# Kernel optimization log

Measured on AMD Instinct MI355X. Metric: run time of the kernel, lower is better.

## Reference

```python
import jax, jax.numpy as jnp
import numpy as np

B, T, C = 2, 2048, 2048
NH = 16          # n_head
G = 4            # group_size
NKV = NH // G    # kv heads
HD = C // NH     # head_dim = 128
BASE = 10000.0


def setup_inputs() -> dict:
    key = jax.random.key(0)
    ks = jax.random.split(key, 9)
    s = 0.02
    return {
        "x": jax.random.normal(ks[0], (B, T, C), jnp.float32),
        "wq_w": jax.random.normal(ks[1], (C, C), jnp.float32) * s,
        "wq_b": jax.random.normal(ks[2], (C,), jnp.float32) * s,
        "wk_w": jax.random.normal(ks[3], (C // G, C), jnp.float32) * s,
        "wk_b": jax.random.normal(ks[4], (C // G,), jnp.float32) * s,
        "wv_w": jax.random.normal(ks[5], (C // G, C), jnp.float32) * s,
        "wv_b": jax.random.normal(ks[6], (C // G,), jnp.float32) * s,
        "cp_w": jax.random.normal(ks[7], (C, C), jnp.float32) * s,
        "cp_b": jax.random.normal(ks[8], (C,), jnp.float32) * s,
    }


def _rope(x):
    # Faithful to source: RoPE is applied to [B, H, T, HD] but the module
    # reads seq_len = x.size(1) == H, so the rotation angle is indexed by the
    # HEAD axis and broadcast over sequence positions.
    b, h, t, d = x.shape
    half = d // 2
    theta = 1.0 / (BASE ** (jnp.arange(0, half, dtype=jnp.float32) * 2.0 / d))  # [half]
    ang = jnp.arange(h, dtype=jnp.float32)[:, None] * theta[None, :]            # [h, half]
    cos = jnp.cos(ang)[None, :, None, :]  # [1, h, 1, half]
    sin = jnp.sin(ang)[None, :, None, :]
    xs = x.reshape(b, h, t, half, 2)
    x0, x1 = xs[..., 0], xs[..., 1]
    out = jnp.stack([x0 * cos - x1 * sin, x1 * cos + x0 * sin], axis=-1)
    return out.reshape(b, h, t, d)


def reference(x, wq_w, wq_b, wk_w, wk_b, wv_w, wv_b, cp_w, cp_b):
    b, t, c = x.shape
    q = x @ wq_w.T + wq_b                                  # [B,T,C]
    k = x @ wk_w.T + wk_b                                  # [B,T,C//G]
    v = x @ wv_w.T + wv_b                                  # [B,T,C//G]
    q = q.reshape(b, t, NH, HD).transpose(0, 2, 1, 3)      # [B,NH,T,HD]
    k = k.reshape(b, t, NKV, HD).transpose(0, 2, 1, 3)     # [B,NKV,T,HD]
    v = v.reshape(b, t, NKV, HD).transpose(0, 2, 1, 3)
    q = _rope(q)
    k = _rope(k)
    # GQA expand: each kv head repeated G times consecutively
    k = jnp.repeat(k, G, axis=1)                           # [B,NH,T,HD]
    v = jnp.repeat(v, G, axis=1)
    att = jnp.einsum('bhqd,bhkd->bhqk', q, k) / (HD ** 0.5)
    mask = jnp.tril(jnp.ones((t, t), dtype=bool))
    att = jnp.where(mask[None, None], att, -jnp.inf)
    att = jax.nn.softmax(att, axis=-1)
    y = jnp.einsum('bhqk,bhkd->bhqd', att, v)
    y = y.transpose(0, 2, 1, 3).reshape(b, t, c)
    return y @ cp_w.T + cp_b
```

## Files before the change

### kernel.cpp

```cpp
#include <hip/hip_runtime.h>

typedef unsigned short u16;
typedef __bf16 bf16x8 __attribute__((ext_vector_type(8)));
typedef float f32x4 __attribute__((ext_vector_type(4)));
typedef float f32x16 __attribute__((ext_vector_type(16)));
typedef unsigned u32x4 __attribute__((ext_vector_type(4)));

#define T_   2048
#define C_   2048
#define HD_  128
#define NH_  16
#define NKV_ 4
#define M_   4096

typedef __attribute__((address_space(1))) const void* as1_cvp;
typedef __attribute__((address_space(3))) void* as3_vp;

__device__ __forceinline__ void gload16(const void* g, void* l) {
  __builtin_amdgcn_global_load_lds((as1_cvp)g, (as3_vp)l, 16, 0, 0);
}

__device__ __forceinline__ u16 f2bf(float f) {
  unsigned u = __builtin_bit_cast(unsigned, f);
  return (u16)((u + 0x7fffu + ((u >> 16) & 1u)) >> 16);
}

__device__ __forceinline__ float fexp2(float x) {
  float r;
  asm("v_exp_f32 %0, %1" : "=v"(r) : "v"(x));
  return r;
}

__device__ __forceinline__ unsigned cvtpk(float a, float b) {
  unsigned d;
  asm("v_cvt_pk_bf16_f32 %0, %1, %2" : "=v"(d) : "v"(a), "v"(b));
  return d;
}

__global__ void cvt_bf16(const float4* __restrict__ in, ushort4* __restrict__ out, int n4) {
  int i = blockIdx.x * blockDim.x + threadIdx.x;
  if (i >= n4) return;
  float4 v = in[i];
  ushort4 r;
  r.x = f2bf(v.x); r.y = f2bf(v.y); r.z = f2bf(v.z); r.w = f2bf(v.w);
  out[i] = r;
}

__global__ void copy_f32(const float* __restrict__ in, float* __restrict__ out, int n) {
  int i = blockIdx.x * blockDim.x + threadIdx.x;
  if (i < n) out[i] = in[i];
}

__global__ void rope_fold_w(const float* __restrict__ W, u16* __restrict__ out, int npair) {
  int idx = blockIdx.x * blockDim.x + threadIdx.x;
  int p  = idx >> 9;
  int c4 = (idx & 511) << 2;
  if (p >= npair) return;
  int h  = p >> 6;
  int ii = p & 63;
  float theta = __expf(-(float)ii * (9.210340371976184f / 64.0f));
  float s, c;
  __sincosf((float)h * theta, &s, &c);
  size_t r0 = (size_t)(2 * p) * 2048 + c4;
  size_t r1 = r0 + 2048;
  float4 a = *(const float4*)(W + r0);
  float4 b = *(const float4*)(W + r1);
  ushort4 o0, o1;
  o0.x = f2bf(a.x * c - b.x * s); o0.y = f2bf(a.y * c - b.y * s);
  o0.z = f2bf(a.z * c - b.z * s); o0.w = f2bf(a.w * c - b.w * s);
  o1.x = f2bf(b.x * c + a.x * s); o1.y = f2bf(b.y * c + a.y * s);
  o1.z = f2bf(b.z * c + a.z * s); o1.w = f2bf(b.w * c + a.w * s);
  *(ushort4*)(out + r0) = o0;
  *(ushort4*)(out + r1) = o1;
}

__global__ void rope_fold_b(const float* __restrict__ bin, float* __restrict__ bout, int npair) {
  int p = blockIdx.x * blockDim.x + threadIdx.x;
  if (p >= npair) return;
  int h = p >> 6, ii = p & 63;
  float theta = __expf(-(float)ii * (9.210340371976184f / 64.0f));
  float s, c;
  __sincosf((float)h * theta, &s, &c);
  float a = bin[2 * p], b = bin[2 * p + 1];
  bout[2 * p]     = a * c - b * s;
  bout[2 * p + 1] = b * c + a * s;
}

template<int BN, int MODE>
__global__ __launch_bounds__(512)
void gemm10(const u16* __restrict__ A, const u16* __restrict__ W,
            const float* __restrict__ bias, void* __restrict__ op0,
            void* __restrict__ op1, void* __restrict__ op2, const float qscale) {
  constexpr int NREP = BN / 32;
  constexpr int ABUF = 16384;
  constexpr int BBUF = BN * 64;
  constexpr int NBL  = BN / 64;
  __shared__ __align__(16) u16 sm[3 * ABUF + 2 * BBUF];
  const int tid  = threadIdx.x;
  const int lane = tid & 63;
  const int wid  = tid >> 6;
  const int wr = wid >> 1, wc = wid & 1;
  const int m0 = blockIdx.y << 8;
  const int n0 = blockIdx.x * BN;
  const int K  = C_;
  const int fr = lane & 15, g = lane >> 4;
  const int rs0 = ((g ^ (fr & 7)) << 3);
  const int rs1 = (((4 + g) ^ (fr & 7)) << 3);

  size_t sofA[4]; int sdstA[4];
#pragma unroll
  for (int l = 0; l < 4; ++l) {
    const int j = l * 512 + tid, rl = j >> 3, sl = j & 7;
    sofA[l] = (size_t)rl * K + ((sl ^ (rl & 7)) << 3);
    sdstA[l] = j * 8;
  }
  size_t sofB[NBL]; int sdstB[NBL];
#pragma unroll
  for (int l = 0; l < NBL; ++l) {
    const int j = l * 512 + tid, rl = j >> 3, sl = j & 7;
    sofB[l] = (size_t)rl * K + ((sl ^ (rl & 7)) << 3);
    sdstB[l] = j * 8;
  }
  const u16* Ab = A + (size_t)m0 * K;
  const u16* Bb = W + (size_t)n0 * K;

  f32x4 acc[4][NREP] = {};

#define SA(l, ks, buf) gload16(Ab + (size_t)(ks) * 64 + sofA[l], sm + (buf) * ABUF + sdstA[l]);
#define SB(l, ks, buf) gload16(Bb + (size_t)(ks) * 64 + sofB[l], sm + 3 * ABUF + (buf) * BBUF + sdstB[l]);
#define LDA(RS) { _Pragma("unroll")                                       \
  for (int mi = 0; mi < 4; ++mi) {                                        \
    const int row = wr * 64 + mi * 16 + fr;                               \
    af[mi] = *(const bf16x8*)&sm[ab + row * 64 + (RS)]; } }
#define LDB(RS) { _Pragma("unroll")                                       \
  for (int ni = 0; ni < NREP; ++ni) {                                     \
    const int row = wc * (BN / 2) + ni * 16 + fr;                         \
    bq[ni] = *(const bf16x8*)&sm[3 * ABUF + bb + row * 64 + (RS)]; } }
#define MMQ { __builtin_amdgcn_s_setprio(1); _Pragma("unroll")            \
  for (int mi = 0; mi < 4; ++mi) _Pragma("unroll")                        \
    for (int ni = 0; ni < NREP; ++ni)                                     \
      acc[mi][ni] = __builtin_amdgcn_mfma_f32_16x16x32_bf16(              \
          af[mi], bq[ni], acc[mi][ni], 0, 0, 0);                          \
  __builtin_amdgcn_s_setprio(0); }
#define LGKM0 { asm volatile("s_waitcnt lgkmcnt(0)" ::: "memory");        \
                __builtin_amdgcn_sched_barrier(0); }

#pragma unroll
  for (int l = 0; l < NBL; ++l) SB(l, 0, 0)
#pragma unroll
  for (int l = 0; l < 4; ++l) SA(l, 0, 0)
#pragma unroll
  for (int l = 0; l < 4; ++l) SA(l, 1, 1)
  asm volatile("s_waitcnt vmcnt(4)" ::: "memory");
  __builtin_amdgcn_s_barrier();

  int a0 = 0, a2 = 2;
  for (int s = 0; s < 32; ++s) {
    const int ab = a0 * ABUF;
    const int bb = (s & 1) * BBUF;
    const int b1 = (s & 1) ^ 1;
    bf16x8 af[4], bq[NREP];
    LDB(rs0) LDA(rs0)
    if (s < 31) {
#pragma unroll
      for (int l = 0; l < NBL; ++l) SB(l, s + 1, b1)
    }
    __builtin_amdgcn_s_barrier();
    LGKM0
    MMQ
    __builtin_amdgcn_s_barrier();
    LDB(rs1) LDA(rs1)
    if (s < 30) {
#pragma unroll
      for (int l = 0; l < 4; ++l) SA(l, s + 2, a2)
      asm volatile("s_waitcnt vmcnt(4)" ::: "memory");
    } else if (s == 30) {
      asm volatile("s_waitcnt vmcnt(0)" ::: "memory");
    }
    __builtin_amdgcn_s_barrier();
    LGKM0
    MMQ
    __builtin_amdgcn_s_barrier();
    a0 = (a0 == 2) ? 0 : a0 + 1;
    a2 = (a2 == 2) ? 0 : a2 + 1;
  }
#undef SA
#undef SB
#undef LDA
#undef LDB
#undef MMQ
#undef LGKM0

#pragma unroll
  for (int mi = 0; mi < 4; ++mi) {
    const int rg0 = m0 + wr * 64 + mi * 16 + ((lane >> 4) << 2);
#pragma unroll
    for (int ni = 0; ni < NREP; ++ni) {
      const int cg = n0 + wc * (BN / 2) + ni * 16 + fr;
      const float bb2 = bias[cg];
#pragma unroll
      for (int r = 0; r < 4; ++r) {
        float v = acc[mi][ni][r] + bb2;
        const int rg = rg0 + r;
        if (MODE == 1) {
          ((float*)op0)[(size_t)rg * C_ + cg] = v;
        } else {
          const int b = rg >> 11, t = rg & (T_ - 1);
          if (cg < 2048) {
            const int h = cg >> 7, d = cg & 127;
            ((u16*)op0)[((((size_t)b * NH_ + h) * T_ + t) << 7) + d] = f2bf(v * qscale);
          } else if (cg < 2560) {
            const int c2 = cg - 2048, h = c2 >> 7, d = c2 & 127;
            ((u16*)op1)[((((size_t)b * NKV_ + h) * T_ + t) << 7) + d] = f2bf(v);
          } else {
            const int c2 = cg - 2560, h = c2 >> 7, d = c2 & 127;
            ((u16*)op2)[(((size_t)b * NKV_ + h) * HD_ + d) * T_ + t] = f2bf(v);
          }
        }
      }
    }
  }
}

__device__ __forceinline__ void stage_kv(u16* dst, const u16* __restrict__ kg,
                                         const u16* __restrict__ vg, int lane, int w) {
#pragma unroll
  for (int r = 0; r < 4; ++r) {
    const int row = r * 16 + w * 4 + (lane >> 4);
    const int cg  = (lane & 15) ^ (row & 7);
    gload16(kg + (size_t)row * 128 + cg * 8, dst + row * 128 + (lane & 15) * 8);
  }
#pragma unroll
  for (int r = 0; r < 4; ++r) {
    const int row = r * 32 + w * 8 + (lane >> 3);
    const int cg  = (lane & 7) ^ (row & 7);
    gload16(vg + (size_t)row * T_ + cg * 8, dst + 8192 + row * 64 + (lane & 7) * 8);
  }
}

__global__ __launch_bounds__(256, 2)
void attn2(const u16* __restrict__ q, const u16* __restrict__ k,
           const u16* __restrict__ vt, u16* __restrict__ y) {
  __shared__ __align__(16) u16 sm[32768];
  const int tid  = threadIdx.x;
  const int lane = tid & 63;
  const int w    = tid >> 6;
  const int hi   = lane >> 5;
  const int l5   = lane & 31;
  const int h = blockIdx.y;
  const int b = blockIdx.z;
  const int qt = b ? (int)blockIdx.x : (15 - (int)blockIdx.x);
  const int q0  = qt << 7;
  const int q0w = q0 + w * 32;
  const int nkv = 2 * qt + 2;
  const size_t qbase = (((size_t)b * NH_ + h) * T_ + q0) * HD_;
  const size_t kbase = ((size_t)b * NKV_ + (h >> 2)) * (size_t)T_ * HD_;
  const size_t vbase = ((size_t)b * NKV_ + (h >> 2)) * (size_t)HD_ * T_;

#pragma unroll
  for (int r = 0; r < 8; ++r) {
    const int row = r * 16 + w * 4 + (lane >> 4);
    const int cg  = (lane & 15) ^ (row & 7);
    gload16(q + qbase + (size_t)row * 128 + cg * 8, sm + row * 128 + (lane & 15) * 8);
  }
  __syncthreads();
  bf16x8 qf[8];
  {
    const int row = w * 32 + l5;
#pragma unroll
    for (int kd = 0; kd < 8; ++kd)
      qf[kd] = *(const bf16x8*)&sm[row * 128 + ((((kd << 1) | hi) ^ (row & 7)) << 3)];
  }
  __syncthreads();
  stage_kv(sm, k + kbase, vt + vbase, lane, w);

  f32x16 o[4] = {};
  float m = -1e30f, l = 0.f;

  for (int kv = 0; kv < nkv; ++kv) {
    __syncthreads();
    const int buf = kv & 1;
    if (kv + 1 < nkv)
      stage_kv(sm + ((buf ^ 1) << 14),
               k + kbase + ((size_t)(kv + 1) << 6) * 128,
               vt + vbase + ((kv + 1) << 6), lane, w);

    if ((kv << 6) <= q0w + 31) {
      const u16* Ks = sm + (buf << 14);
      const u16* Vs = Ks + 8192;

      f32x16 st[2] = {};
      __builtin_amdgcn_s_setprio(1);
#pragma unroll
      for (int kt = 0; kt < 2; ++kt) {
        const int krow = kt * 32 + l5;
#pragma unroll
        for (int kd = 0; kd < 8; ++kd) {
          bf16x8 ka = *(const bf16x8*)&Ks[krow * 128 + ((((kd << 1) | hi) ^ (l5 & 7)) << 3)];
          st[kt] = __builtin_amdgcn_mfma_f32_32x32x16_bf16(ka, qf[kd], st[kt], 0, 0, 0);
        }
      }
      __builtin_amdgcn_s_setprio(0);

      if ((kv << 6) + 63 > q0w) {
        const int qg = q0w + l5;
#pragma unroll
        for (int kt = 0; kt < 2; ++kt)
#pragma unroll
          for (int r = 0; r < 16; ++r) {
            const int kg = (kv << 6) + kt * 32 + (r & 3) + ((r >> 2) << 3) + (hi << 2);
            if (kg > qg) st[kt][r] = -3.0e38f;
          }
      }

      float pmax = -3.0e38f;
#pragma unroll
      for (int kt = 0; kt < 2; ++kt)
#pragma unroll
        for (int r = 0; r < 16; ++r) pmax = fmaxf(pmax, st[kt][r]);
      pmax = fmaxf(pmax, __shfl_xor(pmax, 32));
      if (!__all(pmax - m <= 8.0f)) {
        const float mn = fmaxf(m, pmax);
        const float f = fexp2(m - mn);
        m = mn;
        l *= f;
#pragma unroll
        for (int r = 0; r < 16; ++r) {
          const float fr = __shfl(f, (r & 3) + ((r >> 2) << 3) + (hi << 2));
          o[0][r] *= fr; o[1][r] *= fr; o[2][r] *= fr; o[3][r] *= fr;
        }
      }

      float rs = 0.f;
#pragma unroll
      for (int kt = 0; kt < 2; ++kt) {
#pragma unroll
        for (int s = 0; s < 2; ++s) {
          float e0 = fexp2(st[kt][8 * s + 0] - m), e1 = fexp2(st[kt][8 * s + 1] - m);
          float e2 = fexp2(st[kt][8 * s + 2] - m), e3 = fexp2(st[kt][8 * s + 3] - m);
          float e4 = fexp2(st[kt][8 * s + 4] - m), e5 = fexp2(st[kt][8 * s + 5] - m);
          float e6 = fexp2(st[kt][8 * s + 6] - m), e7 = fexp2(st[kt][8 * s + 7] - m);
          rs += ((e0 + e1) + (e2 + e3)) + ((e4 + e5) + (e6 + e7));
          const unsigned wL0 = cvtpk(e0, e1), wL1 = cvtpk(e2, e3);
          const unsigned wH0 = cvtpk(e4, e5), wH1 = cvtpk(e6, e7);
          const unsigned s0 = hi ? wL0 : wH0, s1 = hi ? wL1 : wH1;
          const unsigned r0 = __shfl_xor(s0, 32), r1 = __shfl_xor(s1, 32);
          u32x4 fw;
          fw.x = hi ? r0 : wL0; fw.y = hi ? r1 : wL1;
          fw.z = hi ? wH0 : r0; fw.w = hi ? wH1 : r1;
          const bf16x8 pa = __builtin_bit_cast(bf16x8, fw);
          const int ch = (((kt * 2 + s) << 1) | hi) ^ (l5 & 7);
          __builtin_amdgcn_s_setprio(1);
#pragma unroll
          for (int ds = 0; ds < 4; ++ds) {
            const int vrow = ds * 32 + l5;
            bf16x8 vb = *(const bf16x8*)&Vs[vrow * 64 + (ch << 3)];
            o[ds] = __builtin_amdgcn_mfma_f32_32x32x16_bf16(pa, vb, o[ds], 0, 0, 0);
          }
          __builtin_amdgcn_s_setprio(0);
        }
      }
      rs += __shfl_xor(rs, 32);
      l += rs;
    }
  }

  const float linv = 1.0f / l;
#pragma unroll
  for (int r = 0; r < 16; ++r) {
    const int crow = (r & 3) + ((r >> 2) << 3) + (hi << 2);
    const float lf = __shfl(linv, crow);
    const int qg = q0w + crow;
    const size_t rowoff = (((size_t)(b << 11) + qg) << 11) + (h << 7) + l5;
#pragma unroll
    for (int ds = 0; ds < 4; ++ds)
      y[rowoff + ds * 32] = f2bf(o[ds][r] * lf);
  }
}

extern "C" void kernel_launch(void* const* d_in, const int* in_sizes, int n_in,
                              void* d_out, int out_size, void* d_ws, size_t ws_size,
                              hipStream_t stream) {
  (void)in_sizes; (void)n_in; (void)out_size; (void)ws_size;
  const float* x    = (const float*)d_in[0];
  const float* wq_w = (const float*)d_in[1];
  const float* wq_b = (const float*)d_in[2];
  const float* wk_w = (const float*)d_in[3];
  const float* wk_b = (const float*)d_in[4];
  const float* wv_w = (const float*)d_in[5];
  const float* wv_b = (const float*)d_in[6];
  const float* cp_w = (const float*)d_in[7];
  const float* cp_b = (const float*)d_in[8];

  char* ws = (char*)d_ws;
  u16* xb  = (u16*)ws;  ws += (size_t)M_ * C_ * 2;
  u16* wqr = (u16*)ws;  ws += (size_t)C_ * C_ * 2;
  u16* wkr = (u16*)ws;  ws += (size_t)512 * C_ * 2;
  u16* wvb = (u16*)ws;  ws += (size_t)512 * C_ * 2;
  u16* cpb = (u16*)ws;  ws += (size_t)C_ * C_ * 2;
  u16* qb  = (u16*)ws;  ws += (size_t)M_ * C_ * 2;
  u16* kb  = (u16*)ws;  ws += (size_t)M_ * 512 * 2;
  u16* vtb = (u16*)ws;  ws += (size_t)M_ * 512 * 2;
  float* bqkv = (float*)ws; ws += 3072 * 4;
  u16* yb = xb;

  cvt_bf16<<<8192, 256, 0, stream>>>((const float4*)x,    (ushort4*)xb,  2097152);
  cvt_bf16<<<1024, 256, 0, stream>>>((const float4*)wv_w, (ushort4*)wvb, 262144);
  cvt_bf16<<<4096, 256, 0, stream>>>((const float4*)cp_w, (ushort4*)cpb, 1048576);
  rope_fold_w<<<2048, 256, 0, stream>>>(wq_w, wqr, 1024);
  rope_fold_w<<<512,  256, 0, stream>>>(wk_w, wkr, 256);
  rope_fold_b<<<4, 256, 0, stream>>>(wq_b, bqkv, 1024);
  rope_fold_b<<<1, 256, 0, stream>>>(wk_b, bqkv + 2048, 256);
  copy_f32<<<2, 256, 0, stream>>>(wv_b, bqkv + 2560, 512);

  const float qscale = 0.08838834764831843f * 1.4426950408889634f;
  gemm10<192, 0><<<dim3(16, 16), 512, 0, stream>>>(xb, wqr, bqkv, qb, kb, vtb, qscale);

  attn2<<<dim3(16, 16, 2), 256, 0, stream>>>(qb, kb, vtb, yb);

  gemm10<128, 1><<<dim3(16, 16), 512, 0, stream>>>(yb, cpb, cp_b, (float*)d_out,
                                                   nullptr, nullptr, 1.0f);
}
```

Baseline: 191.2 us.

## Load both k-halves per stage and use one barrier per GEMM iteration

The GEMM main loop now reads both 32-wide k-halves of the A and B fragments from LDS up front, issues the next global→LDS prefetches, then runs all MFMAs for the stage. The vmcnt wait and a single workgroup barrier move to the end of the iteration, replacing the four barriers and two lgkmcnt waits per iteration. The aim is to cut synchronisation stalls and let LDS reads overlap MFMA work. In exchange it doubles the live fragment registers, which could raise VGPR pressure or cause spills.

```diff
diff --git a/kernel.cpp b/kernel.cpp
--- a/kernel.cpp
+++ b/kernel.cpp
@@ -88,7 +88,7 @@
 
 template<int BN, int MODE>
 __global__ __launch_bounds__(512)
-void gemm10(const u16* __restrict__ A, const u16* __restrict__ W,
+void gemm11(const u16* __restrict__ A, const u16* __restrict__ W,
             const float* __restrict__ bias, void* __restrict__ op0,
             void* __restrict__ op1, void* __restrict__ op2, const float qscale) {
   constexpr int NREP = BN / 32;
@@ -128,22 +128,6 @@
 
 #define SA(l, ks, buf) gload16(Ab + (size_t)(ks) * 64 + sofA[l], sm + (buf) * ABUF + sdstA[l]);
 #define SB(l, ks, buf) gload16(Bb + (size_t)(ks) * 64 + sofB[l], sm + 3 * ABUF + (buf) * BBUF + sdstB[l]);
-#define LDA(RS) { _Pragma("unroll")                                       \
-  for (int mi = 0; mi < 4; ++mi) {                                        \
-    const int row = wr * 64 + mi * 16 + fr;                               \
-    af[mi] = *(const bf16x8*)&sm[ab + row * 64 + (RS)]; } }
-#define LDB(RS) { _Pragma("unroll")                                       \
-  for (int ni = 0; ni < NREP; ++ni) {                                     \
-    const int row = wc * (BN / 2) + ni * 16 + fr;                         \
-    bq[ni] = *(const bf16x8*)&sm[3 * ABUF + bb + row * 64 + (RS)]; } }
-#define MMQ { __builtin_amdgcn_s_setprio(1); _Pragma("unroll")            \
-  for (int mi = 0; mi < 4; ++mi) _Pragma("unroll")                        \
-    for (int ni = 0; ni < NREP; ++ni)                                     \
-      acc[mi][ni] = __builtin_amdgcn_mfma_f32_16x16x32_bf16(              \
-          af[mi], bq[ni], acc[mi][ni], 0, 0, 0);                          \
-  __builtin_amdgcn_s_setprio(0); }
-#define LGKM0 { asm volatile("s_waitcnt lgkmcnt(0)" ::: "memory");        \
-                __builtin_amdgcn_sched_barrier(0); }
 
 #pragma unroll
   for (int l = 0; l < NBL; ++l) SB(l, 0, 0)
@@ -153,43 +137,57 @@
   for (int l = 0; l < 4; ++l) SA(l, 1, 1)
   asm volatile("s_waitcnt vmcnt(4)" ::: "memory");
   __builtin_amdgcn_s_barrier();
+  __builtin_amdgcn_sched_barrier(0);
 
   int a0 = 0, a2 = 2;
   for (int s = 0; s < 32; ++s) {
     const int ab = a0 * ABUF;
-    const int bb = (s & 1) * BBUF;
+    const int bb = 3 * ABUF + (s & 1) * BBUF;
     const int b1 = (s & 1) ^ 1;
-    bf16x8 af[4], bq[NREP];
-    LDB(rs0) LDA(rs0)
+    bf16x8 af0[4], af1[4], bq0[NREP], bq1[NREP];
+#pragma unroll
+    for (int ni = 0; ni < NREP; ++ni)
+      bq0[ni] = *(const bf16x8*)&sm[bb + (wc * (BN / 2) + ni * 16 + fr) * 64 + rs0];
+#pragma unroll
+    for (int mi = 0; mi < 4; ++mi)
+      af0[mi] = *(const bf16x8*)&sm[ab + (wr * 64 + mi * 16 + fr) * 64 + rs0];
+#pragma unroll
+    for (int ni = 0; ni < NREP; ++ni)
+      bq1[ni] = *(const bf16x8*)&sm[bb + (wc * (BN / 2) + ni * 16 + fr) * 64 + rs1];
+#pragma unroll
+    for (int mi = 0; mi < 4; ++mi)
+      af1[mi] = *(const bf16x8*)&sm[ab + (wr * 64 + mi * 16 + fr) * 64 + rs1];
     if (s < 31) {
 #pragma unroll
       for (int l = 0; l < NBL; ++l) SB(l, s + 1, b1)
     }
-    __builtin_amdgcn_s_barrier();
-    LGKM0
-    MMQ
-    __builtin_amdgcn_s_barrier();
-    LDB(rs1) LDA(rs1)
     if (s < 30) {
 #pragma unroll
       for (int l = 0; l < 4; ++l) SA(l, s + 2, a2)
-      asm volatile("s_waitcnt vmcnt(4)" ::: "memory");
-    } else if (s == 30) {
-      asm volatile("s_waitcnt vmcnt(0)" ::: "memory");
     }
-    __builtin_amdgcn_s_barrier();
-    LGKM0
-    MMQ
-    __builtin_amdgcn_s_barrier();
+    __builtin_amdgcn_s_setprio(1);
+#pragma unroll
+    for (int mi = 0; mi < 4; ++mi)
+#pragma unroll
+      for (int ni = 0; ni < NREP; ++ni)
+        acc[mi][ni] = __builtin_amdgcn_mfma_f32_16x16x32_bf16(af0[mi], bq0[ni], acc[mi][ni], 0, 0, 0);
+#pragma unroll
+    for (int mi = 0; mi < 4; ++mi)
+#pragma unroll
+      for (int ni = 0; ni < NREP; ++ni)
+        acc[mi][ni] = __builtin_amdgcn_mfma_f32_16x16x32_bf16(af1[mi], bq1[ni], acc[mi][ni], 0, 0, 0);
+    __builtin_amdgcn_s_setprio(0);
+    if (s < 30)       asm volatile("s_waitcnt vmcnt(4)" ::: "memory");
+    else if (s == 30) asm volatile("s_waitcnt vmcnt(0)" ::: "memory");
+    if (s < 31) {
+      __builtin_amdgcn_s_barrier();
+      __builtin_amdgcn_sched_barrier(0);
+    }
     a0 = (a0 == 2) ? 0 : a0 + 1;
     a2 = (a2 == 2) ? 0 : a2 + 1;
   }
 #undef SA
 #undef SB
-#undef LDA
-#undef LDB
-#undef MMQ
-#undef LGKM0
 
 #pragma unroll
   for (int mi = 0; mi < 4; ++mi) {
@@ -414,10 +412,10 @@
   copy_f32<<<2, 256, 0, stream>>>(wv_b, bqkv + 2560, 512);
 
   const float qscale = 0.08838834764831843f * 1.4426950408889634f;
-  gemm10<192, 0><<<dim3(16, 16), 512, 0, stream>>>(xb, wqr, bqkv, qb, kb, vtb, qscale);
+  gemm11<192, 0><<<dim3(16, 16), 512, 0, stream>>>(xb, wqr, bqkv, qb, kb, vtb, qscale);
 
   attn2<<<dim3(16, 16, 2), 256, 0, stream>>>(qb, kb, vtb, yb);
 
-  gemm10<128, 1><<<dim3(16, 16), 512, 0, stream>>>(yb, cpb, cp_b, (float*)d_out,
+  gemm11<128, 1><<<dim3(16, 16), 512, 0, stream>>>(yb, cpb, cp_b, (float*)d_out,
                                                    nullptr, nullptr, 1.0f);
 }
```

Measured after the change: 187.1 us. 2.2% less time.
